# Kernel optimization log

Measured on AMD Instinct MI355X. Metric: run time of the kernel, lower is better.

Reference implementation:

```python
import jax, jax.numpy as jnp
import numpy as np

B, P = 32, 1024
HID, H, D = 512, 8, 64   # hidden_dim, heads, head_dim
MEM, RANK = 64, 64


def setup_inputs() -> dict:
    key = jax.random.key(0)
    ks = jax.random.split(key, 12)
    s1 = 1.0  # Linear(1, hidden): fan_in = 1 -> torch init bound = 1
    sh = 1.0 / np.sqrt(HID)
    sd = 1.0 / np.sqrt(D)
    return {
        "x":    jax.random.normal(ks[0], (B, P), dtype=jnp.float32),
        # q/k/v: Linear(1, hidden) -> weight (hidden,), bias (hidden,)
        "w_q": jax.random.uniform(ks[1], (HID,), jnp.float32, -s1, s1),
        "b_q": jax.random.uniform(ks[2], (HID,), jnp.float32, -s1, s1),
        "w_k": jax.random.uniform(ks[3], (HID,), jnp.float32, -s1, s1),
        "b_k": jax.random.uniform(ks[4], (HID,), jnp.float32, -s1, s1),
        "w_v": jax.random.uniform(ks[5], (HID,), jnp.float32, -s1, s1),
        "b_v": jax.random.uniform(ks[6], (HID,), jnp.float32, -s1, s1),
        # mem_proj: Linear(head_dim, mem_size, bias=False) -> weight (mem, d)
        "w_mem": jax.random.uniform(ks[7], (MEM, D), jnp.float32, -sd, sd),
        # project_to_U / V: Linear(hidden, rank)
        "w_u":  jax.random.uniform(ks[8], (RANK, HID), jnp.float32, -sh, sh),
        "b_u":  jax.random.uniform(ks[9], (RANK,), jnp.float32, -sh, sh),
        "w_v2": jax.random.uniform(ks[10], (RANK, HID), jnp.float32, -sh, sh),
        "b_v2": jax.random.uniform(ks[11], (RANK,), jnp.float32, -sh, sh),
    }


def reference(x, w_q, b_q, w_k, b_k, w_v, b_v, w_mem, w_u, b_u, w_v2, b_v2):
    Bx, p = x.shape
    xu = x[..., None]                                  # (B, p, 1)
    # Linear(1, hidden) is a scalar broadcast: x * w + b
    def to_heads(w, b):
        y = xu * w + b                                 # (B, p, HID)
        return y.reshape(Bx, p, H, D).transpose(0, 2, 1, 3)  # (B, H, p, D)
    Q = to_heads(w_q, b_q)
    K = to_heads(w_k, b_k)
    V = to_heads(w_v, b_v)

    phi = lambda u: jax.nn.elu(u) + 1.0
    Qf = phi(Q)                                        # (B, H, p, D)
    # memory weights: softmax over the p axis (dim=2)
    W_mem = jax.nn.softmax(jnp.einsum('bhpd,md->bhpm', K, w_mem), axis=2)
    mem_KV = jnp.einsum('bhpm,bhpd->bhmd', W_mem, V)   # (B, H, MEM, D)
    attn = jnp.einsum('bhpd,bhmd->bhpm', Qf, mem_KV)   # (B, H, p, MEM)
    h = jnp.einsum('bhpm,bhmd->bhpd', attn, mem_KV)    # (B, H, p, D)
    h = h.transpose(0, 2, 1, 3).reshape(Bx, p, H * D)  # (B, p, HID)

    U = h @ w_u.T + b_u                                # (B, p, RANK)
    Vp = h @ w_v2.T + b_v2                             # (B, p, RANK)
    coeffs_k = jnp.einsum('bpr,bqr->bpq', U, Vp)       # (B, p, p)
    return coeffs_k
```

## Files before the change

kernel.cpp:

```cpp
#include <hip/hip_runtime.h>
#include <hip/hip_bf16.h>

#define BB 32
#define PP 1024
#define HID 512
#define NH 8
#define DD 64
#define MEM 64
#define RANK 64

#define A_OFF   0
#define M_OFF   512
#define T_OFF   1024
#define S1_OFF  17408
#define S2_OFF  17664
#define G_OFF   18432
#define F_OFF   542720

__global__ __launch_bounds__(1024) void k_precompute(
    const float* __restrict__ wk, const float* __restrict__ wmem,
    const float* __restrict__ wv, const float* __restrict__ bv,
    const float* __restrict__ wu, const float* __restrict__ bu,
    const float* __restrict__ wv2, const float* __restrict__ bv2,
    float* __restrict__ A, float* __restrict__ M17) {
  __shared__ float WU[17 * 64];
  __shared__ float WV[17 * 64];
  const int t = threadIdx.x;

  if (t < 512) {
    const int h = t >> 6, m = t & 63;
    float s = 0.f;
    for (int d = 0; d < DD; ++d) s += wk[h * DD + d] * wmem[m * DD + d];
    A[t] = s;
  }

  for (int i = t; i < 17 * 64; i += 1024) {
    const int j = i >> 6, r = i & 63;
    float su = 0.f, sv = 0.f;
    if (j < 8) {
      for (int d = 0; d < DD; ++d) {
        const float w = wv[j * DD + d];
        su += wu[r * HID + j * DD + d] * w;
        sv += wv2[r * HID + j * DD + d] * w;
      }
    } else if (j < 16) {
      const int h = j - 8;
      for (int d = 0; d < DD; ++d) {
        const float w = bv[h * DD + d];
        su += wu[r * HID + h * DD + d] * w;
        sv += wv2[r * HID + h * DD + d] * w;
      }
    } else {
      su = bu[r];
      sv = bv2[r];
    }
    WU[i] = su;
    WV[i] = sv;
  }
  __syncthreads();

  if (t < 17 * 17) {
    const int i = t / 17, j = t % 17;
    float s = 0.f;
    for (int r = 0; r < 64; ++r) s += WU[i * 64 + r] * WV[j * 64 + r];
    M17[t] = s;
  }
}

__global__ __launch_bounds__(256) void k_memsoftmax(
    const float* __restrict__ x, const float* __restrict__ A,
    float* __restrict__ T) {
  const int wid = blockIdx.x * 4 + (threadIdx.x >> 6);
  const int lane = threadIdx.x & 63;
  const int b = wid >> 9;
  const int hm = wid & 511;
  const float a = A[hm];
  const float* xr = x + b * PP;

  float xs[16];
  float mx = -INFINITY;
#pragma unroll
  for (int k = 0; k < 16; ++k) {
    xs[k] = xr[lane + k * 64];
    mx = fmaxf(mx, xs[k] * a);
  }
#pragma unroll
  for (int off = 32; off >= 1; off >>= 1) mx = fmaxf(mx, __shfl_xor(mx, off));

  float s = 0.f, sx = 0.f;
#pragma unroll
  for (int k = 0; k < 16; ++k) {
    const float e = __expf(xs[k] * a - mx);
    s += e;
    sx += e * xs[k];
  }
#pragma unroll
  for (int off = 32; off >= 1; off >>= 1) {
    s += __shfl_xor(s, off);
    sx += __shfl_xor(sx, off);
  }
  if (lane == 0) T[wid] = sx / s;
}

__global__ __launch_bounds__(256) void k_tsums(
    const float* __restrict__ T, float* __restrict__ S1,
    float* __restrict__ S2) {
  const int t = threadIdx.x;
  const float* Tr = T + t * MEM;
  float s1 = 0.f, s2 = 0.f;
  for (int m = 0; m < MEM; ++m) {
    const float v = Tr[m];
    s1 += v;
    s2 += v * v;
  }
  S1[t] = s1;
  S2[t] = s2;
}

__global__ __launch_bounds__(256) void k_features(
    const float* __restrict__ x, const float* __restrict__ wq,
    const float* __restrict__ bq, const float* __restrict__ wv,
    const float* __restrict__ bv, const float* __restrict__ S1,
    const float* __restrict__ S2, float* __restrict__ G) {
  const int idx0 = blockIdx.x * 256;
  const int b = idx0 >> 13;
  const int h = (idx0 >> 10) & 7;
  const int p = (idx0 & 1023) + threadIdx.x;

  const float xv = x[b * PP + p];
  float a1 = 0.f, a0 = 0.f;
#pragma unroll 8
  for (int d = 0; d < DD; ++d) {
    const float q = xv * wq[h * DD + d] + bq[h * DD + d];
    const float ph = (q > 0.f) ? (q + 1.f) : __expf(q);
    a1 += ph * wv[h * DD + d];
    a0 += ph * bv[h * DD + d];
  }
  const float s1 = S1[b * 8 + h], s2 = S2[b * 8 + h];
  const float c1 = a1 * s2 + a0 * s1;
  const float c2 = a1 * s1 + a0 * (float)MEM;
  G[(b * 16 + h) * PP + p] = c1;
  G[(b * 16 + 8 + h) * PP + p] = c2;
}

__global__ __launch_bounds__(256) void k_fmap(
    const float* __restrict__ G, const float* __restrict__ M17,
    float* __restrict__ F) {
  __shared__ float Ml[17 * 17];
  const int t = threadIdx.x;
  for (int i = t; i < 17 * 17; i += 256) Ml[i] = M17[i];
  __syncthreads();

  const int idx = blockIdx.x * 256 + t;
  const int b = idx >> 10, p = idx & 1023;
  float g[16];
#pragma unroll
  for (int i = 0; i < 16; ++i) g[i] = G[(b * 16 + i) * PP + p];
#pragma unroll
  for (int j = 0; j < 17; ++j) {
    float f = Ml[16 * 17 + j];
#pragma unroll
    for (int i = 0; i < 16; ++i) f += g[i] * Ml[i * 17 + j];
    F[(b * 17 + j) * PP + p] = f;
  }
}

__global__ __launch_bounds__(256) void k_coeffs(
    const float* __restrict__ F, const float* __restrict__ G,
    float* __restrict__ out) {
  __shared__ float Fl[17 * 64];
  __shared__ float Gl[16 * 64];
  const int b = blockIdx.z;
  const int p0 = blockIdx.y * 64;
  const int q0 = blockIdx.x * 64;
  const int t = threadIdx.x;

  const float* Fg = F + (size_t)b * 17 * PP;
  const float* Gg = G + (size_t)b * 16 * PP;
  for (int i = t; i < 17 * 64; i += 256) Fl[i] = Fg[(i >> 6) * PP + p0 + (i & 63)];
  for (int i = t; i < 16 * 64; i += 256) Gl[i] = Gg[(i >> 6) * PP + q0 + (i & 63)];
  __syncthreads();

  const int pr = t >> 4;
  const int qv = t & 15;

  const float4 f16 = *(const float4*)&Fl[16 * 64 + pr * 4];
  float4 acc0 = make_float4(f16.x, f16.x, f16.x, f16.x);
  float4 acc1 = make_float4(f16.y, f16.y, f16.y, f16.y);
  float4 acc2 = make_float4(f16.z, f16.z, f16.z, f16.z);
  float4 acc3 = make_float4(f16.w, f16.w, f16.w, f16.w);

#pragma unroll
  for (int j = 0; j < 16; ++j) {
    const float4 fj = *(const float4*)&Fl[j * 64 + pr * 4];
    const float4 gj = *(const float4*)&Gl[j * 64 + qv * 4];
    acc0.x += fj.x * gj.x; acc0.y += fj.x * gj.y; acc0.z += fj.x * gj.z; acc0.w += fj.x * gj.w;
    acc1.x += fj.y * gj.x; acc1.y += fj.y * gj.y; acc1.z += fj.y * gj.z; acc1.w += fj.y * gj.w;
    acc2.x += fj.z * gj.x; acc2.y += fj.z * gj.y; acc2.z += fj.z * gj.z; acc2.w += fj.z * gj.w;
    acc3.x += fj.w * gj.x; acc3.y += fj.w * gj.y; acc3.z += fj.w * gj.z; acc3.w += fj.w * gj.w;
  }

  const size_t base = ((size_t)(b * PP + p0 + pr * 4)) * PP + q0 + qv * 4;
  *(float4*)&out[base] = acc0;
  *(float4*)&out[base + PP] = acc1;
  *(float4*)&out[base + 2 * PP] = acc2;
  *(float4*)&out[base + 3 * PP] = acc3;
}

extern "C" void kernel_launch(void* const* d_in, const int* in_sizes, int n_in,
                              void* d_out, int out_size, void* d_ws, size_t ws_size,
                              hipStream_t stream) {
  const float* x    = (const float*)d_in[0];
  const float* wq   = (const float*)d_in[1];
  const float* bq   = (const float*)d_in[2];
  const float* wk   = (const float*)d_in[3];
  const float* bk   = (const float*)d_in[4];  (void)bk;
  const float* wv   = (const float*)d_in[5];
  const float* bv   = (const float*)d_in[6];
  const float* wmem = (const float*)d_in[7];
  const float* wu   = (const float*)d_in[8];
  const float* bu   = (const float*)d_in[9];
  const float* wv2  = (const float*)d_in[10];
  const float* bv2  = (const float*)d_in[11];

  float* ws = (float*)d_ws;
  float* A   = ws + A_OFF;
  float* M17 = ws + M_OFF;
  float* T   = ws + T_OFF;
  float* S1  = ws + S1_OFF;
  float* S2  = ws + S2_OFF;
  float* G   = ws + G_OFF;
  float* F   = ws + F_OFF;
  float* out = (float*)d_out;

  k_precompute<<<1, 1024, 0, stream>>>(wk, wmem, wv, bv, wu, bu, wv2, bv2, A, M17);
  k_memsoftmax<<<4096, 256, 0, stream>>>(x, A, T);
  k_tsums<<<1, 256, 0, stream>>>(T, S1, S2);
  k_features<<<1024, 256, 0, stream>>>(x, wq, bq, wv, bv, S1, S2, G);
  k_fmap<<<128, 256, 0, stream>>>(G, M17, F);
  k_coeffs<<<dim3(16, 16, 32), 256, 0, stream>>>(F, G, out);
}
```

Measured before the change: 224.7 us.

## Fuse tsums and fmap into neighbors, enlarge coeffs tile, use nontemporal stores

Removes two small kernel launches by folding the T row sums into k_features (a wave reduction per block) and computing the F feature map inside k_coeffs from a staged G tile. k_coeffs now uses 128x128 output tiles with an 8x8 register micro-tile per thread and writes the output with nontemporal stores. k_precompute is parallelized with float4 loads and shuffle reductions. Recomputing F per tile adds redundant arithmetic and uses more registers, which may lower occupancy. In exchange it drops the F round trip through global memory and the launch overhead.

```diff
diff --git a/kernel.cpp b/kernel.cpp
--- a/kernel.cpp
+++ b/kernel.cpp
@@ -9,13 +9,12 @@
 #define MEM 64
 #define RANK 64
 
+typedef float f32x4 __attribute__((ext_vector_type(4)));
+
 #define A_OFF   0
 #define M_OFF   512
 #define T_OFF   1024
-#define S1_OFF  17408
-#define S2_OFF  17664
 #define G_OFF   18432
-#define F_OFF   542720
 
 __global__ __launch_bounds__(1024) void k_precompute(
     const float* __restrict__ wk, const float* __restrict__ wmem,
@@ -24,45 +23,49 @@
     const float* __restrict__ wv2, const float* __restrict__ bv2,
     float* __restrict__ A, float* __restrict__ M17) {
   __shared__ float WU[17 * 64];
-  __shared__ float WV[17 * 64];
+  __shared__ float WVt[64 * 17];
   const int t = threadIdx.x;
-
-  if (t < 512) {
-    const int h = t >> 6, m = t & 63;
+  const int r = t >> 4;
+  const int dq = t & 15;
+
+  const float4 wm4 = *(const float4*)&wmem[r * DD + dq * 4];
+  for (int h = 0; h < NH; ++h) {
+    const float4 wk4 = *(const float4*)&wk[h * DD + dq * 4];
+    float s = wm4.x * wk4.x + wm4.y * wk4.y + wm4.z * wk4.z + wm4.w * wk4.w;
+    s += __shfl_xor(s, 1); s += __shfl_xor(s, 2);
+    s += __shfl_xor(s, 4); s += __shfl_xor(s, 8);
+    if (dq == 0) A[h * MEM + r] = s;
+  }
+
+  for (int j = 0; j < 17; ++j) {
+    float su, sv;
+    if (j < 16) {
+      const int hh = j & 7;
+      const float4 w4 = (j < 8) ? *(const float4*)&wv[hh * DD + dq * 4]
+                                : *(const float4*)&bv[hh * DD + dq * 4];
+      const float4 u4 = *(const float4*)&wu[r * HID + hh * DD + dq * 4];
+      const float4 v4 = *(const float4*)&wv2[r * HID + hh * DD + dq * 4];
+      su = u4.x * w4.x + u4.y * w4.y + u4.z * w4.z + u4.w * w4.w;
+      sv = v4.x * w4.x + v4.y * w4.y + v4.z * w4.z + v4.w * w4.w;
+    } else {
+      su = (dq == 0) ? bu[r] : 0.f;
+      sv = (dq == 0) ? bv2[r] : 0.f;
+    }
+    su += __shfl_xor(su, 1); su += __shfl_xor(su, 2);
+    su += __shfl_xor(su, 4); su += __shfl_xor(su, 8);
+    sv += __shfl_xor(sv, 1); sv += __shfl_xor(sv, 2);
+    sv += __shfl_xor(sv, 4); sv += __shfl_xor(sv, 8);
+    if (dq == 0) {
+      WU[j * 64 + r] = su;
+      WVt[r * 17 + j] = sv;
+    }
+  }
+  __syncthreads();
+
+  if (t < 17 * 17) {
+    const int ii = t / 17, jj = t - ii * 17;
     float s = 0.f;
-    for (int d = 0; d < DD; ++d) s += wk[h * DD + d] * wmem[m * DD + d];
-    A[t] = s;
-  }
-
-  for (int i = t; i < 17 * 64; i += 1024) {
-    const int j = i >> 6, r = i & 63;
-    float su = 0.f, sv = 0.f;
-    if (j < 8) {
-      for (int d = 0; d < DD; ++d) {
-        const float w = wv[j * DD + d];
-        su += wu[r * HID + j * DD + d] * w;
-        sv += wv2[r * HID + j * DD + d] * w;
-      }
-    } else if (j < 16) {
-      const int h = j - 8;
-      for (int d = 0; d < DD; ++d) {
-        const float w = bv[h * DD + d];
-        su += wu[r * HID + h * DD + d] * w;
-        sv += wv2[r * HID + h * DD + d] * w;
-      }
-    } else {
-      su = bu[r];
-      sv = bv2[r];
-    }
-    WU[i] = su;
-    WV[i] = sv;
-  }
-  __syncthreads();
-
-  if (t < 17 * 17) {
-    const int i = t / 17, j = t % 17;
-    float s = 0.f;
-    for (int r = 0; r < 64; ++r) s += WU[i * 64 + r] * WV[j * 64 + r];
+    for (int rr = 0; rr < 64; ++rr) s += WU[ii * 64 + rr] * WVt[rr * 17 + jj];
     M17[t] = s;
   }
 }
@@ -102,30 +105,28 @@
   if (lane == 0) T[wid] = sx / s;
 }
 
-__global__ __launch_bounds__(256) void k_tsums(
-    const float* __restrict__ T, float* __restrict__ S1,
-    float* __restrict__ S2) {
-  const int t = threadIdx.x;
-  const float* Tr = T + t * MEM;
-  float s1 = 0.f, s2 = 0.f;
-  for (int m = 0; m < MEM; ++m) {
-    const float v = Tr[m];
-    s1 += v;
-    s2 += v * v;
-  }
-  S1[t] = s1;
-  S2[t] = s2;
-}
-
 __global__ __launch_bounds__(256) void k_features(
     const float* __restrict__ x, const float* __restrict__ wq,
     const float* __restrict__ bq, const float* __restrict__ wv,
-    const float* __restrict__ bv, const float* __restrict__ S1,
-    const float* __restrict__ S2, float* __restrict__ G) {
+    const float* __restrict__ bv, const float* __restrict__ T,
+    float* __restrict__ G) {
+  __shared__ float sS1, sS2;
   const int idx0 = blockIdx.x * 256;
   const int b = idx0 >> 13;
   const int h = (idx0 >> 10) & 7;
   const int p = (idx0 & 1023) + threadIdx.x;
+  const int t = threadIdx.x;
+
+  if (t < 64) {
+    const float v = T[(b * NH + h) * MEM + t];
+    float s1 = v, s2 = v * v;
+#pragma unroll
+    for (int off = 32; off >= 1; off >>= 1) {
+      s1 += __shfl_xor(s1, off);
+      s2 += __shfl_xor(s2, off);
+    }
+    if (t == 0) { sS1 = s1; sS2 = s2; }
+  }
 
   const float xv = x[b * PP + p];
   float a1 = 0.f, a0 = 0.f;
@@ -136,75 +137,78 @@
     a1 += ph * wv[h * DD + d];
     a0 += ph * bv[h * DD + d];
   }
-  const float s1 = S1[b * 8 + h], s2 = S2[b * 8 + h];
+  __syncthreads();
+  const float s1 = sS1, s2 = sS2;
   const float c1 = a1 * s2 + a0 * s1;
   const float c2 = a1 * s1 + a0 * (float)MEM;
   G[(b * 16 + h) * PP + p] = c1;
   G[(b * 16 + 8 + h) * PP + p] = c2;
 }
 
-__global__ __launch_bounds__(256) void k_fmap(
+__global__ __launch_bounds__(256) void k_coeffs(
     const float* __restrict__ G, const float* __restrict__ M17,
-    float* __restrict__ F) {
+    float* __restrict__ out) {
   __shared__ float Ml[17 * 17];
+  __shared__ float Gp[16 * 128];
+  __shared__ float Gq[16 * 128];
+  __shared__ float Fl[17 * 128];
+  const int b = blockIdx.z;
+  const int p0 = blockIdx.y * 128;
+  const int q0 = blockIdx.x * 128;
   const int t = threadIdx.x;
+  const float* Gg = G + (size_t)b * 16 * PP;
+
   for (int i = t; i < 17 * 17; i += 256) Ml[i] = M17[i];
-  __syncthreads();
-
-  const int idx = blockIdx.x * 256 + t;
-  const int b = idx >> 10, p = idx & 1023;
-  float g[16];
-#pragma unroll
-  for (int i = 0; i < 16; ++i) g[i] = G[(b * 16 + i) * PP + p];
-#pragma unroll
-  for (int j = 0; j < 17; ++j) {
+  for (int i = t; i < 16 * 128; i += 256) {
+    const int row = i >> 7, col = i & 127;
+    Gp[i] = Gg[row * PP + p0 + col];
+    Gq[i] = Gg[row * PP + q0 + col];
+  }
+  __syncthreads();
+
+  for (int i = t; i < 17 * 128; i += 256) {
+    const int j = i >> 7, pp = i & 127;
     float f = Ml[16 * 17 + j];
 #pragma unroll
-    for (int i = 0; i < 16; ++i) f += g[i] * Ml[i * 17 + j];
-    F[(b * 17 + j) * PP + p] = f;
-  }
-}
-
-__global__ __launch_bounds__(256) void k_coeffs(
-    const float* __restrict__ F, const float* __restrict__ G,
-    float* __restrict__ out) {
-  __shared__ float Fl[17 * 64];
-  __shared__ float Gl[16 * 64];
-  const int b = blockIdx.z;
-  const int p0 = blockIdx.y * 64;
-  const int q0 = blockIdx.x * 64;
-  const int t = threadIdx.x;
-
-  const float* Fg = F + (size_t)b * 17 * PP;
-  const float* Gg = G + (size_t)b * 16 * PP;
-  for (int i = t; i < 17 * 64; i += 256) Fl[i] = Fg[(i >> 6) * PP + p0 + (i & 63)];
-  for (int i = t; i < 16 * 64; i += 256) Gl[i] = Gg[(i >> 6) * PP + q0 + (i & 63)];
+    for (int ii = 0; ii < 16; ++ii) f += Gp[ii * 128 + pp] * Ml[ii * 17 + j];
+    Fl[i] = f;
+  }
   __syncthreads();
 
   const int pr = t >> 4;
   const int qv = t & 15;
 
-  const float4 f16 = *(const float4*)&Fl[16 * 64 + pr * 4];
-  float4 acc0 = make_float4(f16.x, f16.x, f16.x, f16.x);
-  float4 acc1 = make_float4(f16.y, f16.y, f16.y, f16.y);
-  float4 acc2 = make_float4(f16.z, f16.z, f16.z, f16.z);
-  float4 acc3 = make_float4(f16.w, f16.w, f16.w, f16.w);
+  float acc[8][8];
+#pragma unroll
+  for (int r = 0; r < 8; ++r) {
+    const float f16 = Fl[16 * 128 + pr * 8 + r];
+#pragma unroll
+    for (int c = 0; c < 8; ++c) acc[r][c] = f16;
+  }
 
 #pragma unroll
   for (int j = 0; j < 16; ++j) {
-    const float4 fj = *(const float4*)&Fl[j * 64 + pr * 4];
-    const float4 gj = *(const float4*)&Gl[j * 64 + qv * 4];
-    acc0.x += fj.x * gj.x; acc0.y += fj.x * gj.y; acc0.z += fj.x * gj.z; acc0.w += fj.x * gj.w;
-    acc1.x += fj.y * gj.x; acc1.y += fj.y * gj.y; acc1.z += fj.y * gj.z; acc1.w += fj.y * gj.w;
-    acc2.x += fj.z * gj.x; acc2.y += fj.z * gj.y; acc2.z += fj.z * gj.z; acc2.w += fj.z * gj.w;
-    acc3.x += fj.w * gj.x; acc3.y += fj.w * gj.y; acc3.z += fj.w * gj.z; acc3.w += fj.w * gj.w;
-  }
-
-  const size_t base = ((size_t)(b * PP + p0 + pr * 4)) * PP + q0 + qv * 4;
-  *(float4*)&out[base] = acc0;
-  *(float4*)&out[base + PP] = acc1;
-  *(float4*)&out[base + 2 * PP] = acc2;
-  *(float4*)&out[base + 3 * PP] = acc3;
+    const float4 fj0 = *(const float4*)&Fl[j * 128 + pr * 8];
+    const float4 fj1 = *(const float4*)&Fl[j * 128 + pr * 8 + 4];
+    const float4 gj0 = *(const float4*)&Gq[j * 128 + qv * 8];
+    const float4 gj1 = *(const float4*)&Gq[j * 128 + qv * 8 + 4];
+    const float fr[8] = {fj0.x, fj0.y, fj0.z, fj0.w, fj1.x, fj1.y, fj1.z, fj1.w};
+    const float gc[8] = {gj0.x, gj0.y, gj0.z, gj0.w, gj1.x, gj1.y, gj1.z, gj1.w};
+#pragma unroll
+    for (int r = 0; r < 8; ++r) {
+#pragma unroll
+      for (int c = 0; c < 8; ++c) acc[r][c] += fr[r] * gc[c];
+    }
+  }
+
+  const size_t base = ((size_t)b * PP + p0 + pr * 8) * PP + q0 + qv * 8;
+#pragma unroll
+  for (int r = 0; r < 8; ++r) {
+    const f32x4 v0 = {acc[r][0], acc[r][1], acc[r][2], acc[r][3]};
+    const f32x4 v1 = {acc[r][4], acc[r][5], acc[r][6], acc[r][7]};
+    __builtin_nontemporal_store(v0, (f32x4*)&out[base + (size_t)r * PP]);
+    __builtin_nontemporal_store(v1, (f32x4*)&out[base + (size_t)r * PP + 4]);
+  }
 }
 
 extern "C" void kernel_launch(void* const* d_in, const int* in_sizes, int n_in,
@@ -227,16 +231,11 @@
   float* A   = ws + A_OFF;
   float* M17 = ws + M_OFF;
   float* T   = ws + T_OFF;
-  float* S1  = ws + S1_OFF;
-  float* S2  = ws + S2_OFF;
   float* G   = ws + G_OFF;
-  float* F   = ws + F_OFF;
   float* out = (float*)d_out;
 
   k_precompute<<<1, 1024, 0, stream>>>(wk, wmem, wv, bv, wu, bu, wv2, bv2, A, M17);
   k_memsoftmax<<<4096, 256, 0, stream>>>(x, A, T);
-  k_tsums<<<1, 256, 0, stream>>>(T, S1, S2);
-  k_features<<<1024, 256, 0, stream>>>(x, wq, bq, wv, bv, S1, S2, G);
-  k_fmap<<<128, 256, 0, stream>>>(G, M17, F);
-  k_coeffs<<<dim3(16, 16, 32), 256, 0, stream>>>(F, G, out);
-}
+  k_features<<<1024, 256, 0, stream>>>(x, wq, bq, wv, bv, T, G);
+  k_coeffs<<<dim3(8, 8, 32), 256, 0, stream>>>(G, M17, out);
+}
```

Result: faster. 217.3 us (-3.3%).
